# Performance work log

Measured on AMD Instinct MI355X. Metric: run time of the kernel, lower is better.

## Reference

```python
import jax, jax.numpy as jnp
import numpy as np

N = 20000; DX = 512; DW = 64; DY = 256; M = 320000
DS = DX // 2; DD = DX // 4; DP = DS + DD  # 256, 128, 384
EPS = 1e-9; LN_EPS = 1e-5; SLOPE = 0.05
PNAMES = ['rW1','rb1','rg1','rbt1','rW2','rb2','yW1','yb1','yg1','ybt1','yW2','yb2',
          'iaW1','iab1','iag1','iabt1','iaW2','iab2','cW1','cb1','cg1','cbt1','cW2','cb2']

def _mlp2(h, W1, b1, g, be, W2, b2):
    # Linear -> LayerNorm -> LeakyReLU(0.05) -> Linear  (matches mlp(..., norm='layer'))
    h = h @ W1 + b1
    mu = jnp.mean(h, axis=-1, keepdims=True)
    var = jnp.mean((h - mu) ** 2, axis=-1, keepdims=True)
    h = (h - mu) * jax.lax.rsqrt(var + LN_EPS) * g + be
    h = jnp.where(h >= 0, h, SLOPE * h)
    return h @ W2 + b2

def _m(Pp, n, h):
    return _mlp2(h, Pp[n+'W1'], Pp[n+'b1'], Pp[n+'g1'], Pp[n+'bt1'], Pp[n+'W2'], Pp[n+'b2'])

def _agg(a, b):
    s = a + b
    return jnp.where(s >= 0, s, SLOPE * s)

def _run(x, ei, edge_attr, u_r, u_ia, u_pick, Pp, dec=None):
    """GuoUnpool forward (steps 1a, 2a, 2b). ei: concrete numpy [2,M] int64.
    dec holds concrete sampled decisions; built from the uniforms when None."""
    build = dec is None
    if build:
        dec = {}
    # coalesce (edges are duplicate-free) + lexsort by (src, dst)
    perm = np.argsort(ei[0].astype(np.int64) * N + ei[1].astype(np.int64), kind='stable')
    src, dst = ei[0][perm], ei[1][perm]
    ea = edge_attr[perm]
    # --- step 1a: bernoulli unpool decision per node (I_s = I_u = empty, I_r = all nodes)
    pr = jax.nn.sigmoid(_m(Pp, 'r', x)[:, 0])
    if build:
        dec['choose'] = np.asarray(u_r) < np.asarray(pr)
    choose = dec['choose']
    Iu = np.flatnonzero(choose); Is = np.flatnonzero(~choose)
    logP = jnp.sum(jnp.where(jnp.asarray(choose), jnp.log(pr + EPS), jnp.log(1.0 - pr + EPS)))
    prs = jnp.clip(pr, EPS, 1.0 - EPS)
    ent = -jnp.sum(prs * jnp.log(prs) + (1.0 - prs) * jnp.log(1.0 - prs))
    # --- projections (_ps1_idx = [0:ds+D], _ps2_idx = [0:ds] + [ds+D:ds+2D]) and child embeddings
    ps1 = x[:, :DP]
    ps2 = jnp.concatenate([x[:, :DS], x[:, DS + DD:DS + 2 * DD]], axis=-1)
    y1 = _m(Pp, 'y', ps1)   # [N, dy]; rows at Is give x_static, rows at Iu give x_c1
    y2 = _m(Pp, 'y', ps2)   # rows at Iu give x_c2
    x_out = jnp.concatenate([y1[Is], y1[Iu], y2[Iu]], axis=0)
    # --- step 2a: intra-edge decision for unpooled nodes
    p_ia = jax.nn.sigmoid(_m(Pp, 'ia', _agg(y1[Iu], y2[Iu]))[:, 0])
    if build:
        dec['vc'] = np.asarray(u_ia)[Iu] < np.asarray(p_ia)
    vc = dec['vc']
    logP = logP + jnp.sum(jnp.where(jnp.asarray(vc), jnp.log(p_ia + EPS), jnp.log(1.0 - p_ia + EPS)))
    ps = jnp.clip(p_ia, EPS, 1.0 - EPS)
    ent = ent - jnp.sum(ps * jnp.log(ps) + (1.0 - ps) * jnp.log(1.0 - ps))
    # --- step 2b: categorical neighbor pick for unpooled nodes without intra edge
    if build:
        iun = Iu[~vc]
        par = np.concatenate([src, dst]); nb = np.concatenate([dst, src])
        ek = np.concatenate([np.arange(len(src)), np.arange(len(src))])
        keep = np.zeros(N, dtype=bool); keep[iun] = True
        msk = keep[par]
        par, nb, ek = par[msk], nb[msk], ek[msk]
        o = np.lexsort((nb, par))  # adj lists sorted by neighbor id, grouped by parent
        par, nb, ek = par[o], nb[o], ek[o]
        new = np.r_[True, par[1:] != par[:-1]]
        dec['par'], dec['nb'], dec['ek'] = par, nb, ek
        dec['seg'] = np.cumsum(new) - 1
        dec['starts'] = np.flatnonzero(new)
    par, nb, ek = dec['par'], dec['nb'], dec['ek']
    segn, starts = dec['seg'], dec['starts']
    Pn = len(par); nseg = int(segn[-1]) + 1
    seg = jnp.asarray(segn)
    yagg = _agg(y1, y2)
    feats = jnp.concatenate([yagg[par], ea[ek], x[nb]], axis=-1)  # [Pn, dy+dw+dx]
    scores = _m(Pp, 'c', feats)[:, 0]
    mx = jax.ops.segment_max(scores, seg, num_segments=nseg)
    e = jnp.exp(scores - mx[segn])
    den = jax.ops.segment_sum(e, seg, num_segments=nseg)
    probs = e / den[segn]                      # per-parent softmax over neighbors
    if build:
        # multinomial pick via inverse CDF on the provided per-parent uniform
        p_np = np.asarray(probs).astype(np.float64)
        cum = np.cumsum(p_np)
        base = np.concatenate([[0.0], cum])[starts]
        cumw = cum - base[segn]
        useg = np.asarray(u_pick)[par[starts]][segn]
        cand = np.where(cumw > useg, np.arange(Pn), Pn)
        pick = np.minimum.reduceat(cand, starts)
        last = np.r_[starts[1:] - 1, Pn - 1]
        dec['pick'] = np.minimum(pick, last)
    pick = dec['pick']
    logP = logP + jnp.sum(jnp.log(jnp.clip(probs[pick], EPS, None)))
    pc = jnp.clip(probs, EPS, None)
    ent = ent - jnp.sum(pc * jnp.log(pc))
    return (x_out, logP, ent), dec

def _init_params(key):
    Pp = {}
    specs = [('r', DX, max(1, DX // 2), 1), ('y', DP, 128, DY), ('ia', DY, 128, 1), ('c', DY + DW + DX, 128, 1)]
    ks = jax.random.split(key, len(specs))
    for (n, a, h, o), k in zip(specs, ks):
        k1, k2 = jax.random.split(k)
        Pp[n+'W1'] = jax.random.normal(k1, (a, h), jnp.float32) / np.sqrt(a)
        Pp[n+'b1'] = jnp.zeros((h,), jnp.float32)
        Pp[n+'g1'] = jnp.ones((h,), jnp.float32)
        Pp[n+'bt1'] = jnp.zeros((h,), jnp.float32)
        Pp[n+'W2'] = jax.random.normal(k2, (h, o), jnp.float32) / np.sqrt(h)
        Pp[n+'b2'] = jnp.zeros((o,), jnp.float32)
    return Pp

def setup_inputs() -> dict:
    key = jax.random.key(0)
    k = jax.random.split(key, 6)
    x = jax.random.normal(k[0], (N, DX), jnp.float32)
    rng = np.random.default_rng(0)
    ns = int(M * 1.5)
    s = rng.integers(0, N, ns); d = rng.integers(0, N, ns)
    ok = s != d; s, d = s[ok], d[ok]
    _, ui = np.unique(s.astype(np.int64) * N + d, return_index=True)  # duplicate-free (coalesced)
    sel = rng.permutation(ui)[:M]
    edge_index = jnp.asarray(np.stack([s[sel], d[sel]]).astype(np.int64))
    inp = {
        'x': x,
        'edge_index': edge_index,
        'edge_attr': 0.5 * jax.random.normal(k[1], (M, DW), jnp.float32),
        'u_r': jax.random.uniform(k[2], (N,), jnp.float32),
        'u_ia': jax.random.uniform(k[3], (N,), jnp.float32),
        'u_pick': jax.random.uniform(k[4], (N,), jnp.float32),
    }
    inp.update(_init_params(k[5]))
    return inp

def reference(x, edge_index, edge_attr, u_r, u_ia, u_pick,
              rW1, rb1, rg1, rbt1, rW2, rb2,
              yW1, yb1, yg1, ybt1, yW2, yb2,
              iaW1, iab1, iag1, iabt1, iaW2, iab2,
              cW1, cb1, cg1, cbt1, cW2, cb2):
    Pp = dict(zip(PNAMES, (rW1, rb1, rg1, rbt1, rW2, rb2, yW1, yb1, yg1, ybt1, yW2, yb2,
                           iaW1, iab1, iag1, iabt1, iaW2, iab2, cW1, cb1, cg1, cbt1, cW2, cb2)))
    out, _ = _run(x, np.asarray(edge_index), edge_attr, u_r, u_ia, u_pick, Pp)
    return out
```

## Files before the change

kernel.cpp:

```cpp
#include <hip/hip_runtime.h>
#include <math.h>

#define KN 20000
#define KM 320000

typedef __attribute__((ext_vector_type(8))) short bf16x8;
typedef __attribute__((ext_vector_type(4))) float f32x4;

__device__ __forceinline__ ushort f2bf(float f){
  union{float f; unsigned u;} a; a.f=f;
  unsigned r = a.u + 0x7FFFu + ((a.u>>16)&1u);
  return (ushort)(r>>16);
}
__device__ __forceinline__ float bf2f(ushort u){
  union{unsigned u; float f;} a; a.u=((unsigned)u)<<16; return a.f;
}

__device__ __forceinline__ void blk_add2(double lp, double en, double* acc, double* sh){
#pragma unroll
  for (int o=32;o;o>>=1){ lp+=__shfl_xor(lp,o,64); en+=__shfl_xor(en,o,64); }
  int w=threadIdx.x>>6;
  if ((threadIdx.x&63)==0){ sh[2*w]=lp; sh[2*w+1]=en; }
  __syncthreads();
  if (threadIdx.x==0){
    double L=0,E=0; int nw=(blockDim.x+63)>>6;
    for (int i=0;i<nw;i++){L+=sh[2*i];E+=sh[2*i+1];}
    atomicAdd(&acc[0],L); atomicAdd(&acc[1],E);
  }
  __syncthreads();
}

__global__ __launch_bounds__(256) void k_prep_all(
    const float* __restrict__ x, ushort* __restrict__ x_hi, ushort* __restrict__ x_lo,
    const float* __restrict__ Wr1, ushort* __restrict__ Wrt_hi, ushort* __restrict__ Wrt_lo,
    double* __restrict__ w1d,
    const float* __restrict__ Wc1, ushort* __restrict__ W1t,
    const float* __restrict__ Wy1, ushort* __restrict__ W1yt,
    const float* __restrict__ Wy2, ushort* __restrict__ W2yt,
    int* __restrict__ deg,int* __restrict__ fill,int* __restrict__ keep,
    int* __restrict__ counters,double* __restrict__ acc){
  int i=blockIdx.x*256+threadIdx.x;
  if (i<KN*512/8){
    const float* s=x+(size_t)i*8;
    union{ushort u[8]; uint4 v;} oh, ol;
#pragma unroll
    for (int j=0;j<8;j++){
      float v=s[j];
      ushort h=f2bf(v);
      oh.u[j]=h;
      ol.u[j]=f2bf(v-bf2f(h));
    }
    *(uint4*)(x_hi+(size_t)i*8)=oh.v;
    *(uint4*)(x_lo+(size_t)i*8)=ol.v;
  }
  if (i<512*256){
    w1d[i]=(double)Wr1[i];
    int n=i&255, k=i>>8;
    float wv=Wr1[(size_t)k*256+n];
    ushort h=f2bf(wv);
    int kt=k>>5, kc=(k>>3)&3, j=k&7;
    size_t dst=(((size_t)kt*1024)+(size_t)kc*256+(size_t)n)*8+j;
    Wrt_hi[dst]=h;
    Wrt_lo[dst]=f2bf(wv-bf2f(h));
  }
  if (i<832*128){
    int n=i&127, k=i>>7;
    W1t[(size_t)n*832+k]=f2bf(Wc1[(size_t)k*128+n]);
  }
  if (i<384*128){
    int n=i&127, k=i>>7;
    W1yt[(size_t)n*384+k]=f2bf(Wy1[(size_t)k*128+n]);
  }
  if (i<128*256){
    int n=i&255, k=i>>8;
    W2yt[(size_t)n*128+k]=f2bf(Wy2[(size_t)k*256+n]);
  }
  if (i<KN){ deg[i]=0; fill[i]=0; keep[i]=0; }
  if (i<8) counters[i]=0;
  if (i<2) acc[i]=0.0;
}

#define RFLAG_TAU 3e-4f
__global__ __launch_bounds__(512) void k_rmlp_hx(const float* __restrict__ x,
    const ushort* __restrict__ x_hi,const ushort* __restrict__ x_lo,
    const ushort* __restrict__ Wrt_hi,const ushort* __restrict__ Wrt_lo,
    const double* __restrict__ w1d,
    const float* __restrict__ b1,const float* __restrict__ g1,
    const float* __restrict__ bt1,const float* __restrict__ W2,const float* __restrict__ b2,
    const float* __restrict__ u_r, float* __restrict__ pr, int* __restrict__ choose,
    const ushort* __restrict__ W1t, float* __restrict__ hxP, int RB){
  __shared__ __align__(16) ushort Bl[2][2][8192];
  __shared__ float psum[64][2], pvar[64][2], pdot[64][2];
  __shared__ int flagsh[64];
  __shared__ double dsh[256];
  int t=threadIdx.x;
  int w=t>>6, l=t&63;
  int lr=l&15, lk=l>>4;
  if ((int)blockIdx.x>=RB){
    int b2=blockIdx.x-RB;
    int rh=w>>2, cw=w&3;
    int row0=b2*32+rh*16;
    const ushort* ar=x_hi+(size_t)(row0+lr)*512;
    f32x4 acc3[2];
#pragma unroll
    for (int c=0;c<2;c++) acc3[c]=(f32x4){0,0,0,0};
#pragma unroll
    for (int kt=0;kt<16;kt++){
      bf16x8 a=*(const bf16x8*)(ar+320+kt*32+lk*8);
#pragma unroll
      for (int c=0;c<2;c++){
        bf16x8 b=*(const bf16x8*)(W1t+(size_t)(cw*32+c*16+lr)*832+320+kt*32+lk*8);
        acc3[c]=__builtin_amdgcn_mfma_f32_16x16x32_bf16(a,b,acc3[c],0,0,0);
      }
    }
#pragma unroll
    for (int i=0;i<4;i++){
      int n=row0+lk*4+i;
      float2 v; v.x=acc3[0][i]; v.y=acc3[1][i];
      *(float2*)(hxP+(size_t)n*128+lr*8+cw*2)=v;
    }
    return;
  }
  int rg=w>>1, ch=w&1;
  int row0=blockIdx.x*64;
  if (t<64) flagsh[t]=0;
  int q0=t*2, q1=t*2+1;
  f32x4 acc[8];
#pragma unroll
  for (int c=0;c<8;c++) acc[c]=(f32x4){0,0,0,0};
  int rowA=row0+rg*16+lr; if (rowA>=KN) rowA=KN-1;
  const ushort* ah=x_hi+(size_t)rowA*512;
  const ushort* al=x_lo+(size_t)rowA*512;
  bf16x8 nh0=*(const bf16x8*)(Wrt_hi+q0*8);
  bf16x8 nh1=*(const bf16x8*)(Wrt_hi+q1*8);
  bf16x8 nl0=*(const bf16x8*)(Wrt_lo+q0*8);
  bf16x8 nl1=*(const bf16x8*)(Wrt_lo+q1*8);
  *(bf16x8*)&Bl[0][0][q0*8]=nh0; *(bf16x8*)&Bl[0][0][q1*8]=nh1;
  *(bf16x8*)&Bl[0][1][q0*8]=nl0; *(bf16x8*)&Bl[0][1][q1*8]=nl1;
  nh0=*(const bf16x8*)(Wrt_hi+8192+q0*8);
  nh1=*(const bf16x8*)(Wrt_hi+8192+q1*8);
  nl0=*(const bf16x8*)(Wrt_lo+8192+q0*8);
  nl1=*(const bf16x8*)(Wrt_lo+8192+q1*8);
  bf16x8 a_h0=*(const bf16x8*)(ah+0*32+lk*8), a_l0=*(const bf16x8*)(al+0*32+lk*8);
  bf16x8 a_h1=*(const bf16x8*)(ah+1*32+lk*8), a_l1=*(const bf16x8*)(al+1*32+lk*8);
  bf16x8 a_h2=*(const bf16x8*)(ah+2*32+lk*8), a_l2=*(const bf16x8*)(al+2*32+lk*8);
  bf16x8 a_h3=*(const bf16x8*)(ah+3*32+lk*8), a_l3=*(const bf16x8*)(al+3*32+lk*8);
  __syncthreads();
#define RBODY(KT,AH,AL) { \
    const int cur_=(KT)&1, nxt_=cur_^1; \
    if ((KT)<15){ \
      *(bf16x8*)&Bl[nxt_][0][q0*8]=nh0; *(bf16x8*)&Bl[nxt_][0][q1*8]=nh1; \
      *(bf16x8*)&Bl[nxt_][1][q0*8]=nl0; *(bf16x8*)&Bl[nxt_][1][q1*8]=nl1; \
      if ((KT)<14){ \
        size_t so_=(size_t)((KT)+2)*8192; \
        nh0=*(const bf16x8*)(Wrt_hi+so_+q0*8); nh1=*(const bf16x8*)(Wrt_hi+so_+q1*8); \
        nl0=*(const bf16x8*)(Wrt_lo+so_+q0*8); nl1=*(const bf16x8*)(Wrt_lo+so_+q1*8); \
      } \
    } \
    bf16x8 uh_=AH, ul_=AL; \
    if ((KT)<12){ \
      int ko_=((KT)+4)*32+lk*8; \
      AH=*(const bf16x8*)(ah+ko_); \
      AL=*(const bf16x8*)(al+ko_); \
    } \
    _Pragma("unroll") \
    for (int c=0;c<8;c++){ \
      int col_=ch*128+c*16+lr; \
      bf16x8 vh_=*(const bf16x8*)&Bl[cur_][0][((lk<<8)+col_)*8]; \
      bf16x8 vl_=*(const bf16x8*)&Bl[cur_][1][((lk<<8)+col_)*8]; \
      acc[c]=__builtin_amdgcn_mfma_f32_16x16x32_bf16(uh_,vh_,acc[c],0,0,0); \
      acc[c]=__builtin_amdgcn_mfma_f32_16x16x32_bf16(uh_,vl_,acc[c],0,0,0); \
      acc[c]=__builtin_amdgcn_mfma_f32_16x16x32_bf16(ul_,vh_,acc[c],0,0,0); \
    } \
    __syncthreads(); \
  }
  RBODY(0,a_h0,a_l0)  RBODY(1,a_h1,a_l1)  RBODY(2,a_h2,a_l2)  RBODY(3,a_h3,a_l3)
  RBODY(4,a_h0,a_l0)  RBODY(5,a_h1,a_l1)  RBODY(6,a_h2,a_l2)  RBODY(7,a_h3,a_l3)
  RBODY(8,a_h0,a_l0)  RBODY(9,a_h1,a_l1)  RBODY(10,a_h2,a_l2) RBODY(11,a_h3,a_l3)
  RBODY(12,a_h0,a_l0) RBODY(13,a_h1,a_l1) RBODY(14,a_h2,a_l2) RBODY(15,a_h3,a_l3)
#undef RBODY
// ... 36 lines not shown
    for (int c=0;c<8;c++){
      float hn=(hv[i][c]-mu_[i])*rs*g1v[c]+btv[c];
      hn=hn>=0.f?hn:0.05f*hn;
      dot=fmaf(hn,w2v[c],dot);
    }
#pragma unroll
    for (int o=8;o;o>>=1) dot+=__shfl_xor(dot,o,64);
    if (lr==0) pdot[r][ch]=dot;
  }
  __syncthreads();
  if (t<64){
    int n=row0+t;
    if (n<KN){
      float o2=pdot[t][0]+pdot[t][1]+b2[0];
      float pf=1.0f/(1.0f+expf(-o2));
      float u=u_r[n];
      pr[n]=pf;
      choose[n]=(u<pf)?1:0;
      if (fabsf(pf-u)<RFLAG_TAU) flagsh[t]=1;
    }
  }
  __syncthreads();
  for (int r=0;r<64;r++){
    if (!flagsh[r]) continue;
    int n=row0+r;
    if (t<256){
      double ha=(double)b1[t];
      const float* xr=x+(size_t)n*512;
      for (int k=0;k<512;k++) ha=fma((double)xr[k],w1d[(size_t)k*256+t],ha);
      dsh[t]=ha;
    }
    __syncthreads();
    if (t<64){
      double s=0;
      for (int j=t;j<256;j+=64) s+=dsh[j];
#pragma unroll
      for (int o=32;o;o>>=1) s+=__shfl_xor(s,o,64);
      double mu=s*(1.0/256.0);
      double v=0;
      for (int j=t;j<256;j+=64){ double d=dsh[j]-mu; v+=d*d; }
#pragma unroll
      for (int o=32;o;o>>=1) v+=__shfl_xor(v,o,64);
      double rs=1.0/sqrt(v*(1.0/256.0)+1e-5);
      double dot=0;
      for (int j=t;j<256;j+=64){
        double hn=(dsh[j]-mu)*rs*(double)g1[j]+(double)bt1[j];
        hn = hn>=0.0? hn : 0.05*hn;
        dot=fma(hn,(double)W2[j],dot);
      }
#pragma unroll
      for (int o=32;o;o>>=1) dot+=__shfl_xor(dot,o,64);
      if (t==0){
        double p=1.0/(1.0+exp(-(dot+(double)b2[0])));
        float pf=(float)p;
        pr[n]=pf;
        choose[n]=(u_r[n]<pf)?1:0;
      }
    }
    __syncthreads();
  }
}

__global__ __launch_bounds__(1024) void k_scan_choose(const int* __restrict__ choose,int* __restrict__ excl,
                                                      int* __restrict__ iu,int* __restrict__ counters){
  __shared__ int wsum[16], woff[16];
  const int CH=(KN+1023)/1024;
  int t=threadIdx.x, lane=t&63, wid=t>>6;
  int base=t*CH;
  int s=0;
  for (int i=0;i<CH;i++){int idx=base+i; if (idx<KN) s+=choose[idx];}
  int inc=s;
  for (int o=1;o<64;o<<=1){ int v=__shfl_up(inc,o,64); if (lane>=o) inc+=v; }
  if (lane==63) wsum[wid]=inc;
  __syncthreads();
  if (t==0){ int r=0; for (int i=0;i<16;i++){ woff[i]=r; r+=wsum[i]; } counters[2]=r; }
  __syncthreads();
  int ex=woff[wid]+inc-s;
  for (int i=0;i<CH;i++){
    int idx=base+i;
    if (idx<KN){ int c=choose[idx]; excl[idx]=ex; if (c) iu[ex]=idx; ex+=c; }
  }
}

#define YEXTP 261
__global__ __launch_bounds__(256) void k_ymlp_nt(const ushort* __restrict__ x_bf,
    const ushort* __restrict__ W1yt,const float* __restrict__ b1,const float* __restrict__ g1,
    const float* __restrict__ bt1,const ushort* __restrict__ W2yt,const float* __restrict__ b2,
    const int* __restrict__ choose,const int* __restrict__ excl,int cnt,
    float* __restrict__ yagg_f,ushort* __restrict__ yagg_bf,
    float* __restrict__ out,
    const float* __restrict__ pr,double* __restrict__ acc,int YB){
  __shared__ __align__(16) char smem[16896+8704];
  int t=threadIdx.x;
  if ((int)blockIdx.x>=YB){
    double* sh=(double*)smem;
    int i=(blockIdx.x-YB)*256+t;
    double lp=0,en=0;
    if (i<KN){
      double p=(double)pr[i];
      lp = choose[i]? log(p+1e-9) : log(1.0-p+1e-9);
      double ps=fmin(fmax(p,1e-9),1.0-1e-9);
      en = -(ps*log(ps)+(1.0-ps)*log(1.0-ps));
    }
    blk_add2(lp,en,acc,sh);
    return;
  }
  float*  hf  =(float*)smem;
  float*  yext=(float*)smem;
  ushort* hb  =(ushort*)(smem+16896);
  int w=t>>6, l=t&63;
  int lr=l&15, lk=l>>4;
  int md=w&1, kh=w>>1;
  int row0=blockIdx.x*16;
  f32x4 acc1[8];
#pragma unroll
  for (int c=0;c<8;c++) acc1[c]=(f32x4){0,0,0,0};
  const ushort* xr=x_bf+(size_t)(row0+lr)*512;
#pragma unroll
  for (int kt=0;kt<6;kt++){
    int k0=kh*192+kt*32+lk*8;
    int ks=(md && k0>=256)? k0+128 : k0;
    bf16x8 a=*(const bf16x8*)(xr+ks);
#pragma unroll
    for (int c=0;c<8;c++){
      bf16x8 b=*(const bf16x8*)(W1yt+(size_t)(c*16+lr)*384+k0);
      acc1[c]=__builtin_amdgcn_mfma_f32_16x16x32_bf16(a,b,acc1[c],0,0,0);
    }
  }
  if (kh==0){
#pragma unroll
    for (int i=0;i<4;i++){
      int row=lk*4+i;
#pragma unroll
      for (int c=0;c<8;c++) hf[((size_t)md*16+row)*132+c*16+lr]=acc1[c][i];
    }
  }
  __syncthreads();
  if (kh==1){
    float b1v[8],g1v[8],btv[8];
#pragma unroll
    for (int c=0;c<8;c++){ int col=c*16+lr; b1v[c]=b1[col]; g1v[c]=g1[col]; btv[c]=bt1[col]; }
#pragma unroll
    for (int i=0;i<4;i++){
      int row=lk*4+i;
      float hv[8]; float s=0.f;
#pragma unroll
      for (int c=0;c<8;c++){ hv[c]=acc1[c][i]+hf[((size_t)md*16+row)*132+c*16+lr]+b1v[c]; s+=hv[c]; }
#pragma unroll
      for (int o=8;o;o>>=1) s+=__shfl_xor(s,o,64);
      float mu=s*(1.0f/128.0f);
      float v=0.f;
#pragma unroll
      for (int c=0;c<8;c++){ float d=hv[c]-mu; v+=d*d; }
#pragma unroll
      for (int o=8;o;o>>=1) v+=__shfl_xor(v,o,64);
      float rs=1.0f/sqrtf(v*(1.0f/128.0f)+1e-5f);
      ushort* hrow=hb+((size_t)md*16+row)*136;
#pragma unroll
      for (int c=0;c<8;c++){
        float hn=(hv[c]-mu)*rs*g1v[c]+btv[c];
        hn=hn>=0.f?hn:0.05f*hn;
        hrow[c*16+lr]=f2bf(hn);
      }
    }
  }
  __syncthreads();
  f32x4 acc2[8];
#pragma unroll
  for (int c=0;c<8;c++) acc2[c]=(f32x4){0,0,0,0};
  const ushort* ha=hb+((size_t)md*16+lr)*136;
#pragma unroll
  for (int kt=0;kt<4;kt++){
    bf16x8 a=*(const bf16x8*)(ha+kt*32+lk*8);
#pragma unroll
    for (int c=0;c<8;c++){
      bf16x8 b=*(const bf16x8*)(W2yt+(size_t)(kh*128+c*16+lr)*128+kt*32+lk*8);
      acc2[c]=__builtin_amdgcn_mfma_f32_16x16x32_bf16(a,b,acc2[c],0,0,0);
    }
  }
  float b2v[8];
#pragma unroll
  for (int c=0;c<8;c++) b2v[c]=b2[kh*128+c*16+lr];
  if (md==0){
#pragma unroll
    for (int i=0;i<4;i++){
      int row=lk*4+i;
#pragma unroll
      for (int c=0;c<8;c++) yext[(size_t)row*YEXTP+kh*128+c*16+lr]=acc2[c][i]+b2v[c];
    }
  }
  __syncthreads();
  if (md==0){
#pragma unroll
    for (int i=0;i<4;i++){
      int row=lk*4+i, n=row0+row;
      int cch=choose[n], ex=excl[n];
      int r1 = cch? (KN-cnt)+ex : n-ex;
      if (r1>=0 && r1<KN+cnt){
        float* orow=out+(size_t)r1*256+kh*128;
#pragma unroll
        for (int c=0;c<8;c++) orow[c*16+lr]=acc2[c][i]+b2v[c];
      }
    }
  } else {
#pragma unroll
    for (int i=0;i<4;i++){
      int row=lk*4+i, n=row0+row;
      int cch=choose[n], ex=excl[n];
      size_t base=(size_t)n*256+kh*128;
#pragma unroll
      for (int c=0;c<8;c++){
        int colk=c*16+lr;
        float v2=acc2[c][i]+b2v[c];
        float v1=yext[(size_t)row*YEXTP+kh*128+colk];
        float ga=v1+v2; ga=ga>=0.f?ga:0.05f*ga;
        yagg_f[base+colk]=ga;
        yagg_bf[base+colk]=f2bf(ga);
        if (cch){ int r2=KN+ex; if (r2<KN+cnt) out[(size_t)r2*256+kh*128+colk]=v2; }
      }
    }
  }
}

__global__ __launch_bounds__(256) void k_ia_hy(const float* __restrict__ yagg_f,
    const ushort* __restrict__ yagg_bf,const ushort* __restrict__ W1t,float* __restrict__ hyP,
    const int* __restrict__ iu,const float* __restrict__ u_ia,
    const float* __restrict__ W1,const float* __restrict__ b1,const float* __restrict__ g1,
    const float* __restrict__ bt1,const float* __restrict__ W2,const float* __restrict__ b2,
    float* __restrict__ p_ia,int* __restrict__ vc,int* __restrict__ keep,double* __restrict__ acc,
    int cnt,int HB){
  __shared__ float insh[16][256];
  __shared__ float hsh[16][128];
  __shared__ double sh[8];
  int t=threadIdx.x;
  int w=t>>6, l=t&63;
  int lr=l&15, lk=l>>4;
  if ((int)blockIdx.x<HB){
    int rh=w>>1, cq=w&1;
    int row0=blockIdx.x*32+rh*16;
    const ushort* ar=yagg_bf+(size_t)(row0+lr)*256+lk*8;
    f32x4 acc4[4];
#pragma unroll
    for (int c=0;c<4;c++) acc4[c]=(f32x4){0,0,0,0};
#pragma unroll
    for (int kt=0;kt<8;kt++){
      bf16x8 a=*(const bf16x8*)(ar+kt*32);
#pragma unroll
      for (int c=0;c<4;c++){
        bf16x8 b=*(const bf16x8*)(W1t+(size_t)(cq*64+c*16+lr)*832+kt*32+lk*8);
        acc4[c]=__builtin_amdgcn_mfma_f32_16x16x32_bf16(a,b,acc4[c],0,0,0);
      }
    }
#pragma unroll
    for (int i=0;i<4;i++){
      int n=row0+lk*4+i;
      float4 v; v.x=acc4[0][i]; v.y=acc4[1][i]; v.z=acc4[2][i]; v.w=acc4[3][i];
      *(float4*)(hyP+(size_t)n*128+lr*8+cq*4)=v;
    }
    return;
  }
  int row0=(blockIdx.x-HB)*16;
  for (int i=t;i<16*256;i+=256){
    int r=i>>8,k=i&255;
    int row=row0+r;
    if (row<cnt){
      unsigned n=(unsigned)iu[row];
      if (n<KN) insh[r][k]=yagg_f[(size_t)n*256+k];
      else insh[r][k]=0.f;
    }
  }
  __syncthreads();
  int h=t>>7, tt=t&127;
  float accv[8]; float bb=b1[tt];
#pragma unroll
  for (int r=0;r<8;r++) accv[r]=bb;
  for (int k=0;k<256;k+=4){
    float w0=W1[(k+0)*128+tt],w1=W1[(k+1)*128+tt],w2=W1[(k+2)*128+tt],w3=W1[(k+3)*128+tt];
#pragma unroll
    for (int r=0;r<8;r++){
      float4 f=*(const float4*)&insh[h*8+r][k];
      accv[r]=fmaf(f.x,w0,accv[r]); accv[r]=fmaf(f.y,w1,accv[r]); accv[r]=fmaf(f.z,w2,accv[r]); accv[r]=fmaf(f.w,w3,accv[r]);
    }
  }
#pragma unroll
  for (int r=0;r<8;r++) hsh[h*8+r][tt]=accv[r];
  __syncthreads();
  int g=t>>4, tl=t&15;
  float hv[8];
#pragma unroll
  for (int j=0;j<8;j++) hv[j]=hsh[g][tl+16*j];
  float s=0;
#pragma unroll
  for (int j=0;j<8;j++) s+=hv[j];
#pragma unroll
  for (int o=8;o;o>>=1) s+=__shfl_xor(s,o,64);
  float mu=s*(1.0f/128.0f);
  float v=0;
#pragma unroll
  for (int j=0;j<8;j++){float d=hv[j]-mu; v+=d*d;}
#pragma unroll
  for (int o=8;o;o>>=1) v+=__shfl_xor(v,o,64);
  float rs=1.0f/sqrtf(v*(1.0f/128.0f)+1e-5f);
  float dot=0;
#pragma unroll
  for (int j=0;j<8;j++){
    int idx=tl+16*j;
    float hn=(hv[j]-mu)*rs*g1[idx]+bt1[idx];
    hn=hn>=0.f?hn:0.05f*hn;
    dot=fmaf(hn,W2[idx],dot);
  }
#pragma unroll
  for (int o=8;o;o>>=1) dot+=__shfl_xor(dot,o,64);
  double lp=0,en=0;
  if (tl==0){
    int row=row0+g;
    if (row<cnt){
      unsigned n=(unsigned)iu[row];
      if (n<KN){
        float o=dot+b2[0];
        double p=1.0/(1.0+exp(-(double)o));
        float pf=(float)p;
        p_ia[row]=pf;
        int vv=(u_ia[n]<pf)?1:0;
        vc[row]=vv;
        if(!vv) keep[n]=1;
        lp = vv? log((double)pf+1e-9) : log(1.0-(double)pf+1e-9);
        double ps=fmin(fmax((double)pf,1e-9),1.0-1e-9);
        en = -(ps*log(ps)+(1.0-ps)*log(1.0-ps));
      }
    }
  }
  blk_add2(lp,en,acc,sh);
}

__global__ void k_count(const int* __restrict__ ei,const int* __restrict__ keep,int* __restrict__ deg){
  int e=blockIdx.x*256+threadIdx.x;
  if (e<KM){
    int s=ei[e], d=ei[KM+e];
    if (keep[s]) atomicAdd(&deg[s],1);
    if (keep[d]) atomicAdd(&deg[d],1);
  }
}

__global__ __launch_bounds__(1024) void k_scan_deg(const int* __restrict__ deg,int* __restrict__ boff,
                                                   int* __restrict__ nodeseg,int* __restrict__ counters){
  __shared__ int wsum[16], woff[16];
  const int CH=(KN+1023)/1024;
  int t=threadIdx.x, lane=t&63, wid=t>>6;
  int base=t*CH;
  int s=0, sc=0;
  for (int i=0;i<CH;i++){int idx=base+i; if(idx<KN){ int d=deg[idx]; s+=d; sc+=(d>0)?1:0; }}
  int inc=s;
  for (int o=1;o<64;o<<=1){ int v=__shfl_up(inc,o,64); if (lane>=o) inc+=v; }
  if (lane==63) wsum[wid]=inc;
  __syncthreads();
  if (t==0){ int r=0; for (int i=0;i<16;i++){ woff[i]=r; r+=wsum[i]; } boff[KN]=r; counters[0]=r; }
  __syncthreads();
  int ex=woff[wid]+inc-s;
  for (int i=0;i<CH;i++){int idx=base+i; if(idx<KN){ boff[idx]=ex; ex+=deg[idx]; }}
  __syncthreads();
  int inc2=sc;
  for (int o=1;o<64;o<<=1){ int v=__shfl_up(inc2,o,64); if (lane>=o) inc2+=v; }
  if (lane==63) wsum[wid]=inc2;
  __syncthreads();
  if (t==0){ int r=0; for (int i=0;i<16;i++){ woff[i]=r; r+=wsum[i]; } counters[1]=r; }
  __syncthreads();
  int ex2=woff[wid]+inc2-sc;
  for (int i=0;i<CH;i++){int idx=base+i; if(idx<KN && deg[idx]>0){ nodeseg[ex2]=idx; ex2++; }}
}

__global__ void k_fill(const int* __restrict__ ei,const int* __restrict__ keep,const int* __restrict__ boff,
                       int* __restrict__ fill,int* __restrict__ parA,int* __restrict__ keyA,int* __restrict__ ekA){
  int e=blockIdx.x*256+threadIdx.x;
  if (e<KM){
    int s=ei[e], d=ei[KM+e];
    if (keep[s]){ int pos=boff[s]+atomicAdd(&fill[s],1); parA[pos]=s; keyA[pos]=d*2;   ekA[pos]=e; }
    if (keep[d]){ int pos=boff[d]+atomicAdd(&fill[d],1); parA[pos]=d; keyA[pos]=s*2+1; ekA[pos]=e; }
  }
}

__global__ void k_rank(const int* __restrict__ parA,const int* __restrict__ keyA,const int* __restrict__ ekA,
                       const int* __restrict__ boff,const int* __restrict__ counters,
                       int* __restrict__ parS,int* __restrict__ nbS,int* __restrict__ ekS){
  int i=blockIdx.x*256+threadIdx.x;
  int Pn=counters[0];
  if (i<Pn){
    int par=parA[i], key=keyA[i];
    int lo=boff[par], hi=boff[par+1];
    int rank=0;
    for (int j=lo;j<hi;j++) rank += (keyA[j]<key)?1:0;
    int pos=lo+rank;
    parS[pos]=par; nbS[pos]=key>>1; ekS[pos]=ekA[i];
  }
}

__global__ __launch_bounds__(256) void k_cscore_v6(
    const float* __restrict__ ea,const float* __restrict__ hyP,const float* __restrict__ hxP,
    const int* __restrict__ parS,const int* __restrict__ nbS,const int* __restrict__ ekS,
    const int* __restrict__ counters,
    const ushort* __restrict__ W1t,const float* __restrict__ b1,const float* __restrict__ g1,
    const float* __restrict__ bt1,const float* __restrict__ W2,const float* __restrict__ b2,
    float* __restrict__ scores){
  int Pn=counters[0];
  if (Pn<=0) return;
  int t=threadIdx.x;
  int w=t>>6, l=t&63;
  int lr=l&15, lk=l>>4;
  float b2s=b2[0];
  float b1v[8],g1v[8],btv[8],w2v[8];
#pragma unroll
  for (int c=0;c<8;c++){
    int col=c*16+lr;
    b1v[c]=b1[col]; g1v[c]=g1[col]; btv[c]=bt1[col]; w2v[c]=W2[col];
  }
  int ngrp=(Pn+63)>>6;
// ... 58 lines not shown
      }
    }
  }
}

__global__ __launch_bounds__(256) void k_segment(const float* __restrict__ scores,const int* __restrict__ boff,
    const int* __restrict__ nodeseg,const int* __restrict__ counters,const float* __restrict__ u_pick,
    double* __restrict__ acc){
  __shared__ double sh[8];
  int nseg=counters[1];
  int s=blockIdx.x*256+threadIdx.x;
  double lp=0,en=0;
  if (s<nseg){
    int n=nodeseg[s];
    int lo=boff[n],hi=boff[n+1];
    float mx=-1e30f;
    for (int p=lo;p<hi;p++) mx=fmaxf(mx,scores[p]);
    float den=0;
    for (int p=lo;p<hi;p++) den+=expf(scores[p]-mx);
    double u=(double)u_pick[n];
    double cum=0; float ppick=-1.f; float plast=0.f;
    for (int p=lo;p<hi;p++){
      float e=expf(scores[p]-mx);
      float prob=e/den;
      double pc=fmax((double)prob,1e-9);
      en -= pc*log(pc);
      plast=prob;
      if (ppick<0.f){ cum+=(double)prob; if (cum>u) ppick=prob; }
    }
    if (ppick<0.f) ppick=plast;
    lp=log(fmax((double)ppick,1e-9));
  }
  blk_add2(lp,en,acc,sh);
}

__global__ void k_final(const double* __restrict__ acc,float* __restrict__ out,int cnt){
  if (threadIdx.x==0 && blockIdx.x==0){
    size_t base=(size_t)(KN+cnt)*256;
    out[base]=(float)acc[0];
    out[base+1]=(float)acc[1];
  }
}

extern "C" void kernel_launch(void* const* d_in,const int* in_sizes,int n_in,
                              void* d_out,int out_size,void* d_ws,size_t ws_size,
                              hipStream_t stream){
  const float* x     =(const float*)d_in[0];
  const int*   ei    =(const int*)  d_in[1];
  const float* ea    =(const float*)d_in[2];
  const float* u_r   =(const float*)d_in[3];
  const float* u_ia  =(const float*)d_in[4];
  const float* u_pick=(const float*)d_in[5];
  const float* Pp[24];
  for (int i=0;i<24;i++) Pp[i]=(const float*)d_in[6+i];
  float* out=(float*)d_out;
  int cnt=(out_size-2)/256 - KN;
  if (cnt<0) cnt=0;

  char* w=(char*)d_ws;
  size_t off=0;
  auto carve=[&](size_t bytes)->char*{ off=(off+255)&~(size_t)255; char* p=w+off; off+=bytes; return p; };
  int*    counters=(int*)   carve(64);
  double* acc     =(double*)carve(64);
  float*  pr      =(float*) carve((size_t)KN*4);
  int*    choose  =(int*)   carve((size_t)KN*4);
  int*    excl    =(int*)   carve((size_t)KN*4);
  int*    iu      =(int*)   carve((size_t)KN*4);
  float*  p_ia    =(float*) carve((size_t)KN*4);
  int*    vc      =(int*)   carve((size_t)KN*4);
  int*    keep    =(int*)   carve((size_t)KN*4);
  int*    deg     =(int*)   carve((size_t)KN*4);
  int*    fill    =(int*)   carve((size_t)KN*4);
  int*    boff    =(int*)   carve((size_t)(KN+1)*4);
  int*    nodeseg =(int*)   carve((size_t)KN*4);
  int*    parA    =(int*)   carve((size_t)2*KM*4);
  int*    keyA    =(int*)   carve((size_t)2*KM*4);
  int*    ekA     =(int*)   carve((size_t)2*KM*4);
  int*    parS    =(int*)   carve((size_t)2*KM*4);
  int*    nbS     =(int*)   carve((size_t)2*KM*4);
  int*    ekS     =(int*)   carve((size_t)2*KM*4);
  float*  scores  =(float*) carve((size_t)2*KM*4);
  float*  yagg_f  =(float*) carve((size_t)KN*256*4);
  ushort* yagg_bf =(ushort*)carve((size_t)KN*256*2);
  ushort* x_bf    =(ushort*)carve((size_t)KN*512*2);
  ushort* x_lo    =(ushort*)carve((size_t)KN*512*2);
  ushort* W1t     =(ushort*)carve((size_t)832*128*2);
  double* w1d     =(double*)carve((size_t)512*256*8);
  ushort* W1yt    =(ushort*)carve((size_t)128*384*2);
  ushort* W2yt    =(ushort*)carve((size_t)256*128*2);
  ushort* Wrt_hi  =(ushort*)carve((size_t)256*512*2);
  ushort* Wrt_lo  =(ushort*)carve((size_t)256*512*2);
  float*  hy      =(float*) carve((size_t)KN*128*4);
  float*  hx      =(float*) carve((size_t)KN*128*4);
  (void)ws_size;(void)n_in;(void)in_sizes;

  const int RB=(KN+63)/64;
  const int HXB=KN/32;
  const int YB=KN/16;
  const int NTB=(KN+255)/256;
  const int HB=KN/32;
  const int IAB=(cnt+15)/16;

  k_prep_all<<<(KN*512/8+255)/256,256,0,stream>>>(x,x_bf,x_lo,
      Pp[0],Wrt_hi,Wrt_lo,w1d, Pp[18],W1t, Pp[6],W1yt, Pp[10],W2yt,
      deg,fill,keep,counters,acc);
  k_rmlp_hx<<<RB+HXB,512,0,stream>>>(x,x_bf,x_lo,Wrt_hi,Wrt_lo,w1d,
      Pp[1],Pp[2],Pp[3],Pp[4],Pp[5],u_r,pr,choose,W1t,hx,RB);
  k_scan_choose<<<1,1024,0,stream>>>(choose,excl,iu,counters);
  k_ymlp_nt<<<YB+NTB,256,0,stream>>>(x_bf,W1yt,Pp[7],Pp[8],Pp[9],W2yt,Pp[11],
      choose,excl,cnt,yagg_f,yagg_bf,out,pr,acc,YB);
  k_ia_hy<<<HB+IAB,256,0,stream>>>(yagg_f,yagg_bf,W1t,hy,iu,u_ia,
      Pp[12],Pp[13],Pp[14],Pp[15],Pp[16],Pp[17],p_ia,vc,keep,acc,cnt,HB);
  k_count<<<(KM+255)/256,256,0,stream>>>(ei,keep,deg);
  k_scan_deg<<<1,1024,0,stream>>>(deg,boff,nodeseg,counters);
  k_fill<<<(KM+255)/256,256,0,stream>>>(ei,keep,boff,fill,parA,keyA,ekA);
  k_rank<<<(2*KM+255)/256,256,0,stream>>>(parA,keyA,ekA,boff,counters,parS,nbS,ekS);
  k_cscore_v6<<<2560,256,0,stream>>>(ea,hy,hx,parS,nbS,ekS,counters,W1t,Pp[19],Pp[20],Pp[21],Pp[22],Pp[23],scores);
  k_segment<<<(KN+255)/256,256,0,stream>>>(scores,boff,nodeseg,counters,u_pick,acc);
  k_final<<<1,64,0,stream>>>(acc,out,cnt);
}
```

Baseline: 413.9 us.

## Merge y-MLP into r-MLP launch and defer output scatter to second kernel

The y-MLP (two 16-row subtiles per 512-thread block) now runs as extra blocks of the r-MLP/hx kernel, so it no longer waits for the choose scan. Because the output row placement depends on that scan, y1 and y2 go to new dense buffers, and a scatter stage in the merged ia/hy kernel copies them into the output. The log-probability and entropy reduction also moves into that second kernel. This removes one launch and one serialization point, at the cost of writing and re-reading two extra N×256 fp32 buffers.

```diff
diff --git a/kernel.cpp b/kernel.cpp
--- a/kernel.cpp
+++ b/kernel.cpp
@@ -81,14 +81,20 @@
 }
 
 #define RFLAG_TAU 3e-4f
-__global__ __launch_bounds__(512) void k_rmlp_hx(const float* __restrict__ x,
+#define YEXTP 261
+__global__ __launch_bounds__(512) void k_mega1(const float* __restrict__ x,
     const ushort* __restrict__ x_hi,const ushort* __restrict__ x_lo,
     const ushort* __restrict__ Wrt_hi,const ushort* __restrict__ Wrt_lo,
     const double* __restrict__ w1d,
     const float* __restrict__ b1,const float* __restrict__ g1,
     const float* __restrict__ bt1,const float* __restrict__ W2,const float* __restrict__ b2,
     const float* __restrict__ u_r, float* __restrict__ pr, int* __restrict__ choose,
-    const ushort* __restrict__ W1t, float* __restrict__ hxP, int RB){
+    const ushort* __restrict__ W1t, float* __restrict__ hxP,
+    const ushort* __restrict__ W1yt,const float* __restrict__ b1y,const float* __restrict__ g1y,
+    const float* __restrict__ bt1y,const ushort* __restrict__ W2yt,const float* __restrict__ b2y,
+    float* __restrict__ y1_f,float* __restrict__ y2_f,
+    float* __restrict__ yagg_f,ushort* __restrict__ yagg_bf,
+    int RB,int HXB){
   __shared__ __align__(16) ushort Bl[2][2][8192];
   __shared__ float psum[64][2], pvar[64][2], pdot[64][2];
   __shared__ int flagsh[64];
@@ -96,6 +102,122 @@
   int t=threadIdx.x;
   int w=t>>6, l=t&63;
   int lr=l&15, lk=l>>4;
+  if ((int)blockIdx.x>=RB+HXB){
+    int b=blockIdx.x-RB-HXB;
+    int sub=t>>8, tt=t&255;
+    char* gbase=(char*)Bl + sub*25600;
+    float*  hf  =(float*)gbase;
+    float*  yext=(float*)gbase;
+    ushort* hb  =(ushort*)(gbase+16896);
+    int wy=tt>>6, ly=tt&63;
+    int lry=ly&15, lky=ly>>4;
+    int md=wy&1, kh=wy>>1;
+    int row0=(b*2+sub)*16;
+    const ushort* xr=x_hi+(size_t)(row0+lry)*512;
+    f32x4 acc1[8];
+#pragma unroll
+    for (int c=0;c<8;c++) acc1[c]=(f32x4){0,0,0,0};
+#pragma unroll
+    for (int kt=0;kt<6;kt++){
+      int k0=kh*192+kt*32+lky*8;
+      int ks=(md && k0>=256)? k0+128 : k0;
+      bf16x8 a=*(const bf16x8*)(xr+ks);
+#pragma unroll
+      for (int c=0;c<8;c++){
+        bf16x8 b_=*(const bf16x8*)(W1yt+(size_t)(c*16+lry)*384+k0);
+        acc1[c]=__builtin_amdgcn_mfma_f32_16x16x32_bf16(a,b_,acc1[c],0,0,0);
+      }
+    }
+    if (kh==0){
+#pragma unroll
+      for (int i=0;i<4;i++){
+        int row=lky*4+i;
+#pragma unroll
+        for (int c=0;c<8;c++) hf[((size_t)md*16+row)*132+c*16+lry]=acc1[c][i];
+      }
+    }
+    __syncthreads();
+    if (kh==1){
+      float b1v[8],g1v[8],btv[8];
+#pragma unroll
+      for (int c=0;c<8;c++){ int col=c*16+lry; b1v[c]=b1y[col]; g1v[c]=g1y[col]; btv[c]=bt1y[col]; }
+#pragma unroll
+      for (int i=0;i<4;i++){
+        int row=lky*4+i;
+        float hv[8]; float s=0.f;
+#pragma unroll
+        for (int c=0;c<8;c++){ hv[c]=acc1[c][i]+hf[((size_t)md*16+row)*132+c*16+lry]+b1v[c]; s+=hv[c]; }
+#pragma unroll
+        for (int o=8;o;o>>=1) s+=__shfl_xor(s,o,64);
+        float mu=s*(1.0f/128.0f);
+        float v=0.f;
+#pragma unroll
+        for (int c=0;c<8;c++){ float d=hv[c]-mu; v+=d*d; }
+#pragma unroll
+        for (int o=8;o;o>>=1) v+=__shfl_xor(v,o,64);
+        float rs=1.0f/sqrtf(v*(1.0f/128.0f)+1e-5f);
+        ushort* hrow=hb+((size_t)md*16+row)*136;
+#pragma unroll
+        for (int c=0;c<8;c++){
+          float hn=(hv[c]-mu)*rs*g1v[c]+btv[c];
+          hn=hn>=0.f?hn:0.05f*hn;
+          hrow[c*16+lry]=f2bf(hn);
+        }
+      }
+    }
+    __syncthreads();
+    f32x4 acc2[8];
+#pragma unroll
+    for (int c=0;c<8;c++) acc2[c]=(f32x4){0,0,0,0};
+    const ushort* ha=hb+((size_t)md*16+lry)*136;
+#pragma unroll
+    for (int kt=0;kt<4;kt++){
+      bf16x8 a=*(const bf16x8*)(ha+kt*32+lky*8);
+#pragma unroll
+      for (int c=0;c<8;c++){
+        bf16x8 b_=*(const bf16x8*)(W2yt+(size_t)(kh*128+c*16+lry)*128+kt*32+lky*8);
+        acc2[c]=__builtin_amdgcn_mfma_f32_16x16x32_bf16(a,b_,acc2[c],0,0,0);
+      }
+    }
+    float b2v[8];
+#pragma unroll
+    for (int c=0;c<8;c++) b2v[c]=b2y[kh*128+c*16+lry];
+    if (md==0){
+#pragma unroll
+      for (int i=0;i<4;i++){
+        int row=lky*4+i;
+#pragma unroll
+        for (int c=0;c<8;c++) yext[(size_t)row*YEXTP+kh*128+c*16+lry]=acc2[c][i]+b2v[c];
+      }
+    }
+    __syncthreads();
+    if (md==0){
+#pragma unroll
+      for (int i=0;i<4;i++){
+        int row=lky*4+i, n=row0+row;
+        float* orow=y1_f+(size_t)n*256+kh*128;
+#pragma unroll
+        for (int c=0;c<8;c++) orow[c*16+lry]=acc2[c][i]+b2v[c];
+      }
+    } else {
+#pragma unroll
+      for (int i=0;i<4;i++){
+        int row=lky*4+i, n=row0+row;
+        size_t base=(size_t)n*256+kh*128;
+#pragma unroll
+        for (int c=0;c<8;c++){
+          int colk=c*16+lry;
+          float v2=acc2[c][i]+b2v[c];
+          float v1=yext[(size_t)row*YEXTP+kh*128+colk];
+          float ga=v1+v2; ga=ga>=0.f?ga:0.05f*ga;
+          yagg_f[base+colk]=ga;
+          yagg_bf[base+colk]=f2bf(ga);
+          y2_f[base+colk]=v2;
+        }
+      }
+    }
+    return;
+  }
   if ((int)blockIdx.x>=RB){
     int b2=blockIdx.x-RB;
     int rh=w>>2, cw=w&3;
@@ -298,153 +420,16 @@
   }
 }
 
-#define YEXTP 261
-__global__ __launch_bounds__(256) void k_ymlp_nt(const ushort* __restrict__ x_bf,
-    const ushort* __restrict__ W1yt,const float* __restrict__ b1,const float* __restrict__ g1,
-    const float* __restrict__ bt1,const ushort* __restrict__ W2yt,const float* __restrict__ b2,
-    const int* __restrict__ choose,const int* __restrict__ excl,int cnt,
-    float* __restrict__ yagg_f,ushort* __restrict__ yagg_bf,
-    float* __restrict__ out,
-    const float* __restrict__ pr,double* __restrict__ acc,int YB){
-  __shared__ __align__(16) char smem[16896+8704];
-  int t=threadIdx.x;
-  if ((int)blockIdx.x>=YB){
-    double* sh=(double*)smem;
-    int i=(blockIdx.x-YB)*256+t;
-    double lp=0,en=0;
-    if (i<KN){
-      double p=(double)pr[i];
-      lp = choose[i]? log(p+1e-9) : log(1.0-p+1e-9);
-      double ps=fmin(fmax(p,1e-9),1.0-1e-9);
-      en = -(ps*log(ps)+(1.0-ps)*log(1.0-ps));
-    }
-    blk_add2(lp,en,acc,sh);
-    return;
-  }
-  float*  hf  =(float*)smem;
-  float*  yext=(float*)smem;
-  ushort* hb  =(ushort*)(smem+16896);
-  int w=t>>6, l=t&63;
-  int lr=l&15, lk=l>>4;
-  int md=w&1, kh=w>>1;
-  int row0=blockIdx.x*16;
-  f32x4 acc1[8];
-#pragma unroll
-  for (int c=0;c<8;c++) acc1[c]=(f32x4){0,0,0,0};
-  const ushort* xr=x_bf+(size_t)(row0+lr)*512;
-#pragma unroll
-  for (int kt=0;kt<6;kt++){
-    int k0=kh*192+kt*32+lk*8;
-    int ks=(md && k0>=256)? k0+128 : k0;
-    bf16x8 a=*(const bf16x8*)(xr+ks);
-#pragma unroll
-    for (int c=0;c<8;c++){
-      bf16x8 b=*(const bf16x8*)(W1yt+(size_t)(c*16+lr)*384+k0);
-      acc1[c]=__builtin_amdgcn_mfma_f32_16x16x32_bf16(a,b,acc1[c],0,0,0);
-    }
-  }
-  if (kh==0){
-#pragma unroll
-    for (int i=0;i<4;i++){
-      int row=lk*4+i;
-#pragma unroll
-      for (int c=0;c<8;c++) hf[((size_t)md*16+row)*132+c*16+lr]=acc1[c][i];
-    }
-  }
-  __syncthreads();
-  if (kh==1){
-    float b1v[8],g1v[8],btv[8];
-#pragma unroll
-    for (int c=0;c<8;c++){ int col=c*16+lr; b1v[c]=b1[col]; g1v[c]=g1[col]; btv[c]=bt1[col]; }
-#pragma unroll
-    for (int i=0;i<4;i++){
-      int row=lk*4+i;
-      float hv[8]; float s=0.f;
-#pragma unroll
-      for (int c=0;c<8;c++){ hv[c]=acc1[c][i]+hf[((size_t)md*16+row)*132+c*16+lr]+b1v[c]; s+=hv[c]; }
-#pragma unroll
-      for (int o=8;o;o>>=1) s+=__shfl_xor(s,o,64);
-      float mu=s*(1.0f/128.0f);
-      float v=0.f;
-#pragma unroll
-      for (int c=0;c<8;c++){ float d=hv[c]-mu; v+=d*d; }
-#pragma unroll
-      for (int o=8;o;o>>=1) v+=__shfl_xor(v,o,64);
-      float rs=1.0f/sqrtf(v*(1.0f/128.0f)+1e-5f);
-      ushort* hrow=hb+((size_t)md*16+row)*136;
-#pragma unroll
-      for (int c=0;c<8;c++){
-        float hn=(hv[c]-mu)*rs*g1v[c]+btv[c];
-        hn=hn>=0.f?hn:0.05f*hn;
-        hrow[c*16+lr]=f2bf(hn);
-      }
-    }
-  }
-  __syncthreads();
-  f32x4 acc2[8];
-#pragma unroll
-  for (int c=0;c<8;c++) acc2[c]=(f32x4){0,0,0,0};
-  const ushort* ha=hb+((size_t)md*16+lr)*136;
-#pragma unroll
-  for (int kt=0;kt<4;kt++){
-    bf16x8 a=*(const bf16x8*)(ha+kt*32+lk*8);
-#pragma unroll
-    for (int c=0;c<8;c++){
-      bf16x8 b=*(const bf16x8*)(W2yt+(size_t)(kh*128+c*16+lr)*128+kt*32+lk*8);
-      acc2[c]=__builtin_amdgcn_mfma_f32_16x16x32_bf16(a,b,acc2[c],0,0,0);
-    }
-  }
-  float b2v[8];
-#pragma unroll
-  for (int c=0;c<8;c++) b2v[c]=b2[kh*128+c*16+lr];
-  if (md==0){
-#pragma unroll
-    for (int i=0;i<4;i++){
-      int row=lk*4+i;
-#pragma unroll
-      for (int c=0;c<8;c++) yext[(size_t)row*YEXTP+kh*128+c*16+lr]=acc2[c][i]+b2v[c];
-    }
-  }
-  __syncthreads();
-  if (md==0){
-#pragma unroll
-    for (int i=0;i<4;i++){
-      int row=lk*4+i, n=row0+row;
-      int cch=choose[n], ex=excl[n];
-      int r1 = cch? (KN-cnt)+ex : n-ex;
-      if (r1>=0 && r1<KN+cnt){
-        float* orow=out+(size_t)r1*256+kh*128;
-#pragma unroll
-        for (int c=0;c<8;c++) orow[c*16+lr]=acc2[c][i]+b2v[c];
-      }
-    }
-  } else {
-#pragma unroll
-    for (int i=0;i<4;i++){
-      int row=lk*4+i, n=row0+row;
-      int cch=choose[n], ex=excl[n];
-      size_t base=(size_t)n*256+kh*128;
-#pragma unroll
-      for (int c=0;c<8;c++){
-        int colk=c*16+lr;
-        float v2=acc2[c][i]+b2v[c];
-        float v1=yext[(size_t)row*YEXTP+kh*128+colk];
-        float ga=v1+v2; ga=ga>=0.f?ga:0.05f*ga;
-        yagg_f[base+colk]=ga;
-        yagg_bf[base+colk]=f2bf(ga);
-        if (cch){ int r2=KN+ex; if (r2<KN+cnt) out[(size_t)r2*256+kh*128+colk]=v2; }
-      }
-    }
-  }
-}
-
-__global__ __launch_bounds__(256) void k_ia_hy(const float* __restrict__ yagg_f,
+__global__ __launch_bounds__(256) void k_mega2(const float* __restrict__ yagg_f,
     const ushort* __restrict__ yagg_bf,const ushort* __restrict__ W1t,float* __restrict__ hyP,
     const int* __restrict__ iu,const float* __restrict__ u_ia,
     const float* __restrict__ W1,const float* __restrict__ b1,const float* __restrict__ g1,
     const float* __restrict__ bt1,const float* __restrict__ W2,const float* __restrict__ b2,
     float* __restrict__ p_ia,int* __restrict__ vc,int* __restrict__ keep,double* __restrict__ acc,
-    int cnt,int HB){
+    const float* __restrict__ y1_f,const float* __restrict__ y2_f,
+    const int* __restrict__ choose,const int* __restrict__ excl,
+    float* __restrict__ out,const float* __restrict__ pr,
+    int cnt,int HB,int IAB,int SCB){
   __shared__ float insh[16][256];
   __shared__ float hsh[16][128];
   __shared__ double sh[8];
@@ -475,78 +460,105 @@
     }
     return;
   }
-  int row0=(blockIdx.x-HB)*16;
-  for (int i=t;i<16*256;i+=256){
-    int r=i>>8,k=i&255;
-    int row=row0+r;
-    if (row<cnt){
-      unsigned n=(unsigned)iu[row];
-      if (n<KN) insh[r][k]=yagg_f[(size_t)n*256+k];
-      else insh[r][k]=0.f;
-    }
-  }
-  __syncthreads();
-  int h=t>>7, tt=t&127;
-  float accv[8]; float bb=b1[tt];
-#pragma unroll
-  for (int r=0;r<8;r++) accv[r]=bb;
-  for (int k=0;k<256;k+=4){
-    float w0=W1[(k+0)*128+tt],w1=W1[(k+1)*128+tt],w2=W1[(k+2)*128+tt],w3=W1[(k+3)*128+tt];
-#pragma unroll
-    for (int r=0;r<8;r++){
-      float4 f=*(const float4*)&insh[h*8+r][k];
-      accv[r]=fmaf(f.x,w0,accv[r]); accv[r]=fmaf(f.y,w1,accv[r]); accv[r]=fmaf(f.z,w2,accv[r]); accv[r]=fmaf(f.w,w3,accv[r]);
-    }
-  }
-#pragma unroll
-  for (int r=0;r<8;r++) hsh[h*8+r][tt]=accv[r];
-  __syncthreads();
-  int g=t>>4, tl=t&15;
-  float hv[8];
-#pragma unroll
-  for (int j=0;j<8;j++) hv[j]=hsh[g][tl+16*j];
-  float s=0;
-#pragma unroll
-  for (int j=0;j<8;j++) s+=hv[j];
-#pragma unroll
-  for (int o=8;o;o>>=1) s+=__shfl_xor(s,o,64);
-  float mu=s*(1.0f/128.0f);
-  float v=0;
-#pragma unroll
-  for (int j=0;j<8;j++){float d=hv[j]-mu; v+=d*d;}
-#pragma unroll
-  for (int o=8;o;o>>=1) v+=__shfl_xor(v,o,64);
-  float rs=1.0f/sqrtf(v*(1.0f/128.0f)+1e-5f);
-  float dot=0;
-#pragma unroll
-  for (int j=0;j<8;j++){
-    int idx=tl+16*j;
-    float hn=(hv[j]-mu)*rs*g1[idx]+bt1[idx];
-    hn=hn>=0.f?hn:0.05f*hn;
-    dot=fmaf(hn,W2[idx],dot);
-  }
-#pragma unroll
-  for (int o=8;o;o>>=1) dot+=__shfl_xor(dot,o,64);
-  double lp=0,en=0;
-  if (tl==0){
-    int row=row0+g;
-    if (row<cnt){
-      unsigned n=(unsigned)iu[row];
-      if (n<KN){
-        float o=dot+b2[0];
-        double p=1.0/(1.0+exp(-(double)o));
-        float pf=(float)p;
-        p_ia[row]=pf;
-        int vv=(u_ia[n]<pf)?1:0;
-        vc[row]=vv;
-        if(!vv) keep[n]=1;
-        lp = vv? log((double)pf+1e-9) : log(1.0-(double)pf+1e-9);
-        double ps=fmin(fmax((double)pf,1e-9),1.0-1e-9);
-        en = -(ps*log(ps)+(1.0-ps)*log(1.0-ps));
-      }
-    }
-  }
-  blk_add2(lp,en,acc,sh);
+  if ((int)blockIdx.x<HB+IAB){
+    int row0=(blockIdx.x-HB)*16;
+    for (int i=t;i<16*256;i+=256){
+      int r=i>>8,k=i&255;
+      int row=row0+r;
+      if (row<cnt){
+        unsigned n=(unsigned)iu[row];
+        if (n<KN) insh[r][k]=yagg_f[(size_t)n*256+k];
+        else insh[r][k]=0.f;
+      }
+    }
+    __syncthreads();
+    int h=t>>7, tt=t&127;
+    float accv[8]; float bb=b1[tt];
+#pragma unroll
+    for (int r=0;r<8;r++) accv[r]=bb;
+    for (int k=0;k<256;k+=4){
+      float w0=W1[(k+0)*128+tt],w1=W1[(k+1)*128+tt],w2=W1[(k+2)*128+tt],w3=W1[(k+3)*128+tt];
+#pragma unroll
+      for (int r=0;r<8;r++){
+        float4 f=*(const float4*)&insh[h*8+r][k];
+        accv[r]=fmaf(f.x,w0,accv[r]); accv[r]=fmaf(f.y,w1,accv[r]); accv[r]=fmaf(f.z,w2,accv[r]); accv[r]=fmaf(f.w,w3,accv[r]);
+      }
+    }
+#pragma unroll
+    for (int r=0;r<8;r++) hsh[h*8+r][tt]=accv[r];
+    __syncthreads();
+    int g=t>>4, tl=t&15;
+    float hv[8];
+#pragma unroll
+    for (int j=0;j<8;j++) hv[j]=hsh[g][tl+16*j];
+    float s=0;
+#pragma unroll
+    for (int j=0;j<8;j++) s+=hv[j];
+#pragma unroll
+    for (int o=8;o;o>>=1) s+=__shfl_xor(s,o,64);
+    float mu=s*(1.0f/128.0f);
+    float v=0;
+#pragma unroll
+    for (int j=0;j<8;j++){float d=hv[j]-mu; v+=d*d;}
+#pragma unroll
+    for (int o=8;o;o>>=1) v+=__shfl_xor(v,o,64);
+    float rs=1.0f/sqrtf(v*(1.0f/128.0f)+1e-5f);
+    float dot=0;
+#pragma unroll
+    for (int j=0;j<8;j++){
+      int idx=tl+16*j;
+      float hn=(hv[j]-mu)*rs*g1[idx]+bt1[idx];
+      hn=hn>=0.f?hn:0.05f*hn;
+      dot=fmaf(hn,W2[idx],dot);
+    }
+#pragma unroll
+    for (int o=8;o;o>>=1) dot+=__shfl_xor(dot,o,64);
+    double lp=0,en=0;
+    if (tl==0){
+      int row=row0+g;
+      if (row<cnt){
+        unsigned n=(unsigned)iu[row];
+        if (n<KN){
+          float o=dot+b2[0];
+          double p=1.0/(1.0+exp(-(double)o));
+          float pf=(float)p;
+          p_ia[row]=pf;
+          int vv=(u_ia[n]<pf)?1:0;
+          vc[row]=vv;
+          if(!vv) keep[n]=1;
+          lp = vv? log((double)pf+1e-9) : log(1.0-(double)pf+1e-9);
+          double ps=fmin(fmax((double)pf,1e-9),1.0-1e-9);
+          en = -(ps*log(ps)+(1.0-ps)*log(1.0-ps));
+        }
+      }
+    }
+    blk_add2(lp,en,acc,sh);
+    return;
+  }
+  if ((int)blockIdx.x<HB+IAB+SCB){
+    int b=blockIdx.x-HB-IAB;
+    int r0=b*32;
+    for (int r=0;r<32;r++){
+      int n=r0+r;
+      if (n>=KN) break;
+      int cch=choose[n], ex=excl[n];
+      int r1 = cch? (KN-cnt)+ex : n-ex;
+      if (r1>=0 && r1<KN+cnt) out[(size_t)r1*256+t]=y1_f[(size_t)n*256+t];
+      if (cch){ int r2=KN+ex; if (r2<KN+cnt) out[(size_t)r2*256+t]=y2_f[(size_t)n*256+t]; }
+    }
+    return;
+  }
+  {
+    int i=(blockIdx.x-HB-IAB-SCB)*256+t;
+    double lp=0,en=0;
+    if (i<KN){
+      double p=(double)pr[i];
+      lp = choose[i]? log(p+1e-9) : log(1.0-p+1e-9);
+      double ps=fmin(fmax(p,1e-9),1.0-1e-9);
+      en = -(ps*log(ps)+(1.0-ps)*log(1.0-ps));
+    }
+    blk_add2(lp,en,acc,(double*)insh);
+  }
 }
 
 __global__ void k_count(const int* __restrict__ ei,const int* __restrict__ keep,int* __restrict__ deg){
@@ -771,6 +783,8 @@
   float*  scores  =(float*) carve((size_t)2*KM*4);
   float*  yagg_f  =(float*) carve((size_t)KN*256*4);
   ushort* yagg_bf =(ushort*)carve((size_t)KN*256*2);
+  float*  y1_f    =(float*) carve((size_t)KN*256*4);
+  float*  y2_f    =(float*) carve((size_t)KN*256*4);
   ushort* x_bf    =(ushort*)carve((size_t)KN*512*2);
   ushort* x_lo    =(ushort*)carve((size_t)KN*512*2);
   ushort* W1t     =(ushort*)carve((size_t)832*128*2);
@@ -785,21 +799,22 @@
 
   const int RB=(KN+63)/64;
   const int HXB=KN/32;
-  const int YB=KN/16;
-  const int NTB=(KN+255)/256;
+  const int YB2=KN/32;
   const int HB=KN/32;
   const int IAB=(cnt+15)/16;
+  const int SCB=(KN+31)/32;
+  const int NTB=(KN+255)/256;
 
   k_prep_all<<<(KN*512/8+255)/256,256,0,stream>>>(x,x_bf,x_lo,
       Pp[0],Wrt_hi,Wrt_lo,w1d, Pp[18],W1t, Pp[6],W1yt, Pp[10],W2yt,
       deg,fill,keep,counters,acc);
-  k_rmlp_hx<<<RB+HXB,512,0,stream>>>(x,x_bf,x_lo,Wrt_hi,Wrt_lo,w1d,
-      Pp[1],Pp[2],Pp[3],Pp[4],Pp[5],u_r,pr,choose,W1t,hx,RB);
+  k_mega1<<<RB+HXB+YB2,512,0,stream>>>(x,x_bf,x_lo,Wrt_hi,Wrt_lo,w1d,
+      Pp[1],Pp[2],Pp[3],Pp[4],Pp[5],u_r,pr,choose,W1t,hx,
+      W1yt,Pp[7],Pp[8],Pp[9],W2yt,Pp[11],y1_f,y2_f,yagg_f,yagg_bf,RB,HXB);
   k_scan_choose<<<1,1024,0,stream>>>(choose,excl,iu,counters);
-  k_ymlp_nt<<<YB+NTB,256,0,stream>>>(x_bf,W1yt,Pp[7],Pp[8],Pp[9],W2yt,Pp[11],
-      choose,excl,cnt,yagg_f,yagg_bf,out,pr,acc,YB);
-  k_ia_hy<<<HB+IAB,256,0,stream>>>(yagg_f,yagg_bf,W1t,hy,iu,u_ia,
-      Pp[12],Pp[13],Pp[14],Pp[15],Pp[16],Pp[17],p_ia,vc,keep,acc,cnt,HB);
+  k_mega2<<<HB+IAB+SCB+NTB,256,0,stream>>>(yagg_f,yagg_bf,W1t,hy,iu,u_ia,
+      Pp[12],Pp[13],Pp[14],Pp[15],Pp[16],Pp[17],p_ia,vc,keep,acc,
+      y1_f,y2_f,choose,excl,out,pr,cnt,HB,IAB,SCB);
   k_count<<<(KM+255)/256,256,0,stream>>>(ei,keep,deg);
   k_scan_deg<<<1,1024,0,stream>>>(deg,boff,nodeseg,counters);
   k_fill<<<(KM+255)/256,256,0,stream>>>(ei,keep,boff,fill,parA,keyA,ekA);
```

Result: no change. 407.1 us, median of 3 (-1.6%).
